# Performance work log

Measured on AMD Instinct MI355X. Metric: run time of the kernel, lower is better.

Reference implementation:

```python
import jax, jax.numpy as jnp
import numpy as np

TEMP = 0.5   # temperature from __init__
EPS = 1e-8   # torch.nn.CosineSimilarity eps


def setup_inputs() -> dict:
    key = jax.random.key(0)
    N, D = 8192, 256
    x = jax.random.normal(key, (N, D), dtype=jnp.float32)
    # pairs: each label appears exactly twice, as required for the
    # sim[~mask].reshape(N, -1) in the original to be well-formed
    y = jnp.arange(N, dtype=jnp.int32) // 2
    return {"x": x, "y": y}


def reference(x, y):
    # cosine similarity matrix: normalize once, then one NxD @ DxN matmul
    # (equivalent to CosineSimilarity(x.unsqueeze(1), x.unsqueeze(0)) without
    #  the NxNxD intermediate)
    norm = jnp.maximum(jnp.linalg.norm(x, axis=1, keepdims=True), EPS)
    xn = x / norm
    sim = (xn @ xn.T) / TEMP                     # [N, N]

    # Original: positives = equal-label entries (row-major order, includes the
    # diagonal), logits = [positives | negatives] which is just a per-row
    # permutation of sim; labels = 0 -> CE target is the FIRST equal-label
    # column of each row. logsumexp is over the full row (all N entries).
    eq = y[:, None] == y[None, :]                # [N, N] bool
    first_pos = jnp.argmax(eq, axis=1)           # first column j with y_j == y_i
    target = jnp.take_along_axis(sim, first_pos[:, None], axis=1)[:, 0]  # [N]

    lse = jax.nn.logsumexp(sim, axis=1)          # [N]
    N = x.shape[0]
    loss = jnp.sum(lse - target) / N             # CrossEntropyLoss(sum) / N
    return loss
```

## Files before the change

### kernel.cpp

```cpp
#include <hip/hip_runtime.h>
#include <hip/hip_bf16.h>

#define D 256
#define INV_TEMP 2.0f

typedef __attribute__((ext_vector_type(8))) short short8;
typedef __attribute__((ext_vector_type(4))) float floatx4;

__device__ __forceinline__ unsigned short f2bf(float f) {
    union { float f; unsigned u; } a; a.f = f;
    unsigned r = (a.u + 0x7fffu + ((a.u >> 16) & 1u)) >> 16;
    return (unsigned short)r;
}

__device__ __forceinline__ void gload_lds16(const unsigned short* g,
                                            unsigned short* l) {
    __builtin_amdgcn_global_load_lds(
        (const __attribute__((address_space(1))) unsigned int*)g,
        (__attribute__((address_space(3))) unsigned int*)l, 16, 0, 0);
}

__global__ void nt_prep_kernel(const float* __restrict__ x,
                               unsigned short* __restrict__ xnb,
                               float* __restrict__ pair_dot,
                               float* __restrict__ gsum,
                               unsigned int* __restrict__ gcnt) {
    if (blockIdx.x == 0 && threadIdx.x == 0) { *gsum = 0.f; *gcnt = 0u; }
    int p    = blockIdx.x * 4 + (threadIdx.x >> 6);
    int lane = threadIdx.x & 63;
    const float4* a4 = (const float4*)(x + (size_t)(2 * p) * D);
    const float4* b4 = (const float4*)(x + (size_t)(2 * p + 1) * D);
    float4 a = a4[lane], b = b4[lane];
    float saa = a.x * a.x + a.y * a.y + a.z * a.z + a.w * a.w;
    float sbb = b.x * b.x + b.y * b.y + b.z * b.z + b.w * b.w;
    float sab = a.x * b.x + a.y * b.y + a.z * b.z + a.w * b.w;
    #pragma unroll
    for (int off = 32; off; off >>= 1) {
        saa += __shfl_xor(saa, off);
        sbb += __shfl_xor(sbb, off);
        sab += __shfl_xor(sab, off);
    }
    float inva = 1.0f / fmaxf(sqrtf(saa), 1e-8f);
    float invb = 1.0f / fmaxf(sqrtf(sbb), 1e-8f);
    ushort4 oa, ob;
    oa.x = f2bf(a.x * inva); oa.y = f2bf(a.y * inva);
    oa.z = f2bf(a.z * inva); oa.w = f2bf(a.w * inva);
    ob.x = f2bf(b.x * invb); ob.y = f2bf(b.y * invb);
    ob.z = f2bf(b.z * invb); ob.w = f2bf(b.w * invb);
    ((ushort4*)(xnb + (size_t)(2 * p) * D))[lane] = oa;
    ((ushort4*)(xnb + (size_t)(2 * p + 1) * D))[lane] = ob;
    if (lane == 0)
        pair_dot[p] = sab * inva * invb * INV_TEMP;
}

__global__ __launch_bounds__(256, 2)
void nt_simexp_kernel(const unsigned short* __restrict__ xnb,
                      float* __restrict__ contrib) {
    __shared__ __align__(16) unsigned short Bs[128 * 256];

    const int p  = blockIdx.x >> 4, q = blockIdx.x & 15;
    const int s1 = 63 - p;
    const int c0 = 64 - p;
    const int q0 = (p + q) & 15;

    const int tid  = threadIdx.x;
    const int wave = tid >> 6, lane = tid & 63;
    const int wm   = wave & 1, wn = wave >> 1;
    const int quad = lane >> 4, c = lane & 15;

    auto strip_of = [&](int i) { return (i < c0) ? p : s1; };
    auto bi_of    = [&](int i) { return (i < c0) ? (p + i) : (s1 + i - c0); };

    auto load_B = [&](int bj) {
        const unsigned short* src = xnb + (size_t)(bj * 128) * D;
        int rs = lane >> 5, pp = lane & 31;
        #pragma unroll
        for (int t = 0; t < 16; ++t) {
            int wl = wave * 16 + t;
            int rr = wl * 2 + rs;
            int j  = (pp & ~7) | ((pp ^ rr) & 7);
            gload_lds16(src + (size_t)rr * D + j * 8, Bs + wl * 512 + lane * 8);
        }
    };

    short8 abuf[2][4], bbuf[2][4];

    auto load_a = [&](short8* dst, int bi, int ph) {
        const unsigned short* src = xnb + (size_t)(bi * 128 + wm * 64 + c) * D
                                        + ph * 32 + quad * 8;
        #pragma unroll
        for (int mt = 0; mt < 4; ++mt)
            dst[mt] = *(const short8*)(src + mt * 16 * D);
    };
    auto load_b = [&](short8* dst, int ph) {
        const int jg = ph * 4 + quad;
        const int pB = (jg & ~7) | ((jg ^ c) & 7);
        #pragma unroll
        for (int nt = 0; nt < 4; ++nt)
            dst[nt] = *(const short8*)(Bs + (wn * 64 + nt * 16 + c) * D + pB * 8);
    };

    floatx4 acc[4][4];

    int bj = strip_of(q0);
    load_B(bj);
    load_a(abuf[0], bi_of(q0), 0);
    __syncthreads();
    load_b(bbuf[0], 0);

    for (int i = q0; i < 65; i += 16) {
        const int bi = bi_of(i);
        const int ni = i + 16;
        const bool have_next = (ni < 65);
        const int nbj = have_next ? strip_of(ni) : -1;
        const bool same = have_next && (nbj == bj);

        #pragma unroll
        for (int mt = 0; mt < 4; ++mt)
            #pragma unroll
            for (int nt = 0; nt < 4; ++nt)
                acc[mt][nt] = (floatx4){0.f, 0.f, 0.f, 0.f};

        #pragma unroll
        for (int ph = 0; ph < 8; ++ph) {
            const int cur = ph & 1, nxt = cur ^ 1;
            if (ph < 7) {
                load_a(abuf[nxt], bi, ph + 1);
                load_b(bbuf[nxt], ph + 1);
            } else if (same) {
                load_a(abuf[0], bi_of(ni), 0);
                load_b(bbuf[0], 0);
            }
            #pragma unroll
            for (int mt = 0; mt < 4; ++mt)
                #pragma unroll
                for (int nt = 0; nt < 4; ++nt)
                    acc[mt][nt] = __builtin_amdgcn_mfma_f32_16x16x32_bf16(
                        abuf[cur][mt], bbuf[cur][nt], acc[mt][nt], 0, 0, 0);
        }

        if (have_next && !same) {
            __syncthreads();
            load_B(nbj);
            load_a(abuf[0], bi_of(ni), 0);
        }

        #pragma unroll
        for (int mt = 0; mt < 4; ++mt)
            #pragma unroll
            for (int nt = 0; nt < 4; ++nt)
                #pragma unroll
                for (int r = 0; r < 4; ++r)
                    acc[mt][nt][r] = __expf(acc[mt][nt][r] * INV_TEMP);

        #pragma unroll
        for (int mt = 0; mt < 4; ++mt) {
            float ps[4] = {0.f, 0.f, 0.f, 0.f};
            #pragma unroll
            for (int nt = 0; nt < 4; ++nt)
                #pragma unroll
                for (int r = 0; r < 4; ++r)
                    ps[r] += acc[mt][nt][r];
            #pragma unroll
            for (int off = 1; off < 16; off <<= 1)
                #pragma unroll
                for (int r = 0; r < 4; ++r)
                    ps[r] += __shfl_xor(ps[r], off);
            if (c == 0) {
                float4 v = {ps[0], ps[1], ps[2], ps[3]};
                *(float4*)(contrib + (((size_t)bi * 64 + bj) * 2 + wn) * 128 +
                           wm * 64 + mt * 16 + quad * 4) = v;
            }
        }
        if (bi != bj) {
            #pragma unroll
            for (int nt = 0; nt < 4; ++nt) {
                float cs = 0.f;
                #pragma unroll
                for (int mt = 0; mt < 4; ++mt)
                    #pragma unroll
                    for (int r = 0; r < 4; ++r)
                        cs += acc[mt][nt][r];
                cs += __shfl_xor(cs, 16);
                cs += __shfl_xor(cs, 32);
                if (quad == 0)
                    contrib[(((size_t)bj * 64 + bi) * 2 + wm) * 128 +
                            wn * 64 + nt * 16 + c] = cs;
            }
        }
        if (have_next && !same) {
            __syncthreads();
            bj = nbj;
            load_b(bbuf[0], 0);
        }
    }
}

__global__ void nt_reduce_kernel(const float* __restrict__ contrib,
                                 const float* __restrict__ pair_dot,
                                 float* __restrict__ gsum,
                                 unsigned int* __restrict__ gcnt,
                                 float* __restrict__ out, int N) {
    __shared__ float sm[256];
    __shared__ __align__(16) float rs[2][128];
    int b  = blockIdx.x;
    int jp = threadIdx.x & 3;
    int idx = threadIdx.x >> 2;
    int h  = idx >> 5, rg = idx & 31;
    const float* base = contrib + (((size_t)b * 64 + jp) * 2 + h) * 128 + rg * 4;
    float4 s = {0.f, 0.f, 0.f, 0.f};
    #pragma unroll
    for (int j16 = 0; j16 < 16; ++j16) {
        float4 v = *(const float4*)(base + (size_t)j16 * 1024);
        s.x += v.x; s.y += v.y; s.z += v.z; s.w += v.w;
    }
    #pragma unroll
    for (int off = 1; off < 4; off <<= 1) {
        s.x += __shfl_xor(s.x, off);
        s.y += __shfl_xor(s.y, off);
        s.z += __shfl_xor(s.z, off);
        s.w += __shfl_xor(s.w, off);
    }
    if (jp == 0) {
        float4 v = {s.x, s.y, s.z, s.w};
        *(float4*)&rs[h][rg * 4] = v;
    }
    __syncthreads();
    float v = 0.f;
    int rl = threadIdx.x & 127;
    if (threadIdx.x < 128) v = logf(rs[0][rl] + rs[1][rl]);
    else if (rl < 64)      v = -pair_dot[b * 64 + rl];
    sm[threadIdx.x] = v;
    __syncthreads();
    for (int st = 128; st; st >>= 1) {
        if ((int)threadIdx.x < st) sm[threadIdx.x] += sm[threadIdx.x + st];
        __syncthreads();
    }
    if (threadIdx.x == 0) {
        atomicAdd(gsum, sm[0]);
        __threadfence();
        if (atomicAdd(gcnt, 1u) == 63u) {
            __threadfence();
            float tot = atomicAdd(gsum, 0.0f);
            out[0] = (tot - (float)N) / (float)N;
        }
    }
}

extern "C" void kernel_launch(void* const* d_in, const int* in_sizes, int n_in,
                              void* d_out, int out_size, void* d_ws, size_t ws_size,
                              hipStream_t stream) {
    const float* x = (const float*)d_in[0];
    int N = in_sizes[0] / D;

    char* ws = (char*)d_ws;
    unsigned short* xnb = (unsigned short*)ws;
    float* pair_dot  = (float*)(ws + (size_t)N * D * 2);
    float* contrib   = pair_dot + N / 2;
    float* gsum      = contrib + (size_t)64 * 64 * 2 * 128;
    unsigned int* gcnt = (unsigned int*)(gsum + 1);

    nt_prep_kernel<<<N / 8, 256, 0, stream>>>(x, xnb, pair_dot, gsum, gcnt);
    nt_simexp_kernel<<<512, 256, 0, stream>>>(xnb, contrib);
    nt_reduce_kernel<<<N / 128, 256, 0, stream>>>(contrib, pair_dot, gsum, gcnt,
                                                  (float*)d_out, N);
}
```

Baseline: 113.8 us.

## Stage A tiles through LDS with a 4-deep async pipeline and 256-row blocks

The sim-exp kernel now uses 512-thread blocks that compute 256x128 tiles. A-operand k-slices are staged into a 4-buffer LDS ring via global_load_lds with a swizzled layout, replacing direct per-wave global loads, and explicit vmcnt waits plus barriers overlap loads with MFMA. The triangular tile schedule is rebuilt for 256-row A tiles, and the diagonal is handled per 128-row half. MFMA sections get raised wave priority. The intent is better reuse of A across waves and hidden load latency, at the cost of more LDS (occupancy), more barriers, and a larger grid granularity of 256 blocks.

```diff
diff --git a/kernel.cpp b/kernel.cpp
--- a/kernel.cpp
+++ b/kernel.cpp
@@ -53,67 +53,89 @@
         pair_dot[p] = sab * inva * invb * INV_TEMP;
 }
 
-__global__ __launch_bounds__(256, 2)
+__global__ __launch_bounds__(512, 2)
 void nt_simexp_kernel(const unsigned short* __restrict__ xnb,
                       float* __restrict__ contrib) {
     __shared__ __align__(16) unsigned short Bs[128 * 256];
-
-    const int p  = blockIdx.x >> 4, q = blockIdx.x & 15;
-    const int s1 = 63 - p;
-    const int c0 = 64 - p;
-    const int q0 = (p + q) & 15;
+    __shared__ __align__(16) unsigned short As[4][256 * 32];
+
+    const int p  = blockIdx.x >> 3, q = blockIdx.x & 7;
+    const int n0 = 32 - (p >> 1);
+    const int q0 = (p + q) & 7;
 
     const int tid  = threadIdx.x;
     const int wave = tid >> 6, lane = tid & 63;
-    const int wm   = wave & 1, wn = wave >> 1;
+    const int wm   = wave & 3, wn = wave >> 2;
     const int quad = lane >> 4, c = lane & 15;
-
-    auto strip_of = [&](int i) { return (i < c0) ? p : s1; };
-    auto bi_of    = [&](int i) { return (i < c0) ? (p + i) : (s1 + i - c0); };
+    const int pA   = quad ^ ((c >> 1) & 3);
+
+    auto bj_of = [&](int t) { return (t < n0) ? p : 63 - p; };
+    auto a_of  = [&](int t) { return (t < n0) ? (p >> 1) + t
+                                              : ((63 - p) >> 1) + (t - n0); };
 
     auto load_B = [&](int bj) {
         const unsigned short* src = xnb + (size_t)(bj * 128) * D;
         int rs = lane >> 5, pp = lane & 31;
         #pragma unroll
-        for (int t = 0; t < 16; ++t) {
-            int wl = wave * 16 + t;
+        for (int t = 0; t < 8; ++t) {
+            int wl = wave * 8 + t;
             int rr = wl * 2 + rs;
             int j  = (pp & ~7) | ((pp ^ rr) & 7);
             gload_lds16(src + (size_t)rr * D + j * 8, Bs + wl * 512 + lane * 8);
         }
     };
-
-    short8 abuf[2][4], bbuf[2][4];
-
-    auto load_a = [&](short8* dst, int bi, int ph) {
-        const unsigned short* src = xnb + (size_t)(bi * 128 + wm * 64 + c) * D
-                                        + ph * 32 + quad * 8;
-        #pragma unroll
-        for (int mt = 0; mt < 4; ++mt)
-            dst[mt] = *(const short8*)(src + mt * 16 * D);
+    auto load_A = [&](int a, int ph, unsigned short* Ab) {
+        const unsigned short* src = xnb + (size_t)(a * 256) * D + ph * 32;
+        int rl = lane >> 2, pq = lane & 3;
+        #pragma unroll
+        for (int t = 0; t < 2; ++t) {
+            int wl = wave * 2 + t;
+            int rr = wl * 16 + rl;
+            int j  = pq ^ ((rr >> 1) & 3);
+            gload_lds16(src + (size_t)rr * D + j * 8, Ab + wl * 512 + lane * 8);
+        }
     };
-    auto load_b = [&](short8* dst, int ph) {
+
+    floatx4 acc[4][4];
+    auto compute = [&](const unsigned short* Ab, int ph) {
+        short8 af[4], bf[4];
+        #pragma unroll
+        for (int mt = 0; mt < 4; ++mt)
+            af[mt] = *(const short8*)(Ab + (wm * 64 + mt * 16 + c) * 32 + pA * 8);
         const int jg = ph * 4 + quad;
         const int pB = (jg & ~7) | ((jg ^ c) & 7);
         #pragma unroll
         for (int nt = 0; nt < 4; ++nt)
-            dst[nt] = *(const short8*)(Bs + (wn * 64 + nt * 16 + c) * D + pB * 8);
+            bf[nt] = *(const short8*)(Bs + (wn * 64 + nt * 16 + c) * 256 + pB * 8);
+        __builtin_amdgcn_s_setprio(1);
+        #pragma unroll
+        for (int mt = 0; mt < 4; ++mt)
+            #pragma unroll
+            for (int nt = 0; nt < 4; ++nt)
+                acc[mt][nt] = __builtin_amdgcn_mfma_f32_16x16x32_bf16(
+                    af[mt], bf[nt], acc[mt][nt], 0, 0, 0);
+        __builtin_amdgcn_s_setprio(0);
     };
 
-    floatx4 acc[4][4];
-
-    int bj = strip_of(q0);
+    int t0 = q0;
+    int bj = bj_of(t0);
     load_B(bj);
-    load_a(abuf[0], bi_of(q0), 0);
-    __syncthreads();
-    load_b(bbuf[0], 0);
-
-    for (int i = q0; i < 65; i += 16) {
-        const int bi = bi_of(i);
-        const int ni = i + 16;
-        const bool have_next = (ni < 65);
-        const int nbj = have_next ? strip_of(ni) : -1;
-        const bool same = have_next && (nbj == bj);
+    {
+        int a0 = a_of(t0);
+        load_A(a0, 0, As[0]);
+        load_A(a0, 1, As[1]);
+        load_A(a0, 2, As[2]);
+    }
+    asm volatile("s_waitcnt vmcnt(4)" ::: "memory");
+    __builtin_amdgcn_s_barrier();
+    asm volatile("" ::: "memory");
+
+    for (int t = t0; t < 33; t += 8) {
+        const int a  = a_of(t);
+        const int tn = t + 8;
+        const bool have_next = (tn < 33);
+        const int a_next  = have_next ? a_of(tn) : 0;
+        const int bj_next = have_next ? bj_of(tn) : -1;
 
         #pragma unroll
         for (int mt = 0; mt < 4; ++mt)
@@ -122,28 +144,23 @@
                 acc[mt][nt] = (floatx4){0.f, 0.f, 0.f, 0.f};
 
         #pragma unroll
-        for (int ph = 0; ph < 8; ++ph) {
-            const int cur = ph & 1, nxt = cur ^ 1;
-            if (ph < 7) {
-                load_a(abuf[nxt], bi, ph + 1);
-                load_b(bbuf[nxt], ph + 1);
-            } else if (same) {
-                load_a(abuf[0], bi_of(ni), 0);
-                load_b(bbuf[0], 0);
+        for (int lp = 0; lp < 8; ++lp) {
+            if (lp < 5)           load_A(a,      lp + 3, As[(lp + 3) & 3]);
+            else if (have_next)   load_A(a_next, lp - 5, As[(lp + 3) & 3]);
+
+            compute(As[lp & 3], lp);
+
+            if (lp < 5 || have_next) {
+                asm volatile("s_waitcnt vmcnt(4)" ::: "memory");
+            } else if (lp < 7) {
+                asm volatile("s_waitcnt vmcnt(0)" ::: "memory");
             }
-            #pragma unroll
-            for (int mt = 0; mt < 4; ++mt)
-                #pragma unroll
-                for (int nt = 0; nt < 4; ++nt)
-                    acc[mt][nt] = __builtin_amdgcn_mfma_f32_16x16x32_bf16(
-                        abuf[cur][mt], bbuf[cur][nt], acc[mt][nt], 0, 0, 0);
-        }
-
-        if (have_next && !same) {
-            __syncthreads();
-            load_B(nbj);
-            load_a(abuf[0], bi_of(ni), 0);
-        }
+            __builtin_amdgcn_s_barrier();
+            asm volatile("" ::: "memory");
+        }
+
+        const int bi128 = 2 * a + (wm >> 1);
+        const int hrow  = wm & 1;
 
         #pragma unroll
         for (int mt = 0; mt < 4; ++mt)
@@ -153,26 +170,29 @@
                 for (int r = 0; r < 4; ++r)
                     acc[mt][nt][r] = __expf(acc[mt][nt][r] * INV_TEMP);
 
-        #pragma unroll
-        for (int mt = 0; mt < 4; ++mt) {
-            float ps[4] = {0.f, 0.f, 0.f, 0.f};
-            #pragma unroll
-            for (int nt = 0; nt < 4; ++nt)
-                #pragma unroll
-                for (int r = 0; r < 4; ++r)
-                    ps[r] += acc[mt][nt][r];
-            #pragma unroll
-            for (int off = 1; off < 16; off <<= 1)
-                #pragma unroll
-                for (int r = 0; r < 4; ++r)
-                    ps[r] += __shfl_xor(ps[r], off);
-            if (c == 0) {
-                float4 v = {ps[0], ps[1], ps[2], ps[3]};
-                *(float4*)(contrib + (((size_t)bi * 64 + bj) * 2 + wn) * 128 +
-                           wm * 64 + mt * 16 + quad * 4) = v;
+        if (bi128 >= bj) {
+            #pragma unroll
+            for (int mt = 0; mt < 4; ++mt) {
+                float ps[4] = {0.f, 0.f, 0.f, 0.f};
+                #pragma unroll
+                for (int nt = 0; nt < 4; ++nt)
+                    #pragma unroll
+                    for (int r = 0; r < 4; ++r)
+                        ps[r] += acc[mt][nt][r];
+                #pragma unroll
+                for (int off = 1; off < 16; off <<= 1)
+                    #pragma unroll
+                    for (int r = 0; r < 4; ++r)
+                        ps[r] += __shfl_xor(ps[r], off);
+                if (c == 0) {
+                    float4 v = {ps[0], ps[1], ps[2], ps[3]};
+                    *(float4*)(contrib +
+                        (((size_t)bi128 * 64 + bj) * 2 + wn) * 128 +
+                        hrow * 64 + mt * 16 + quad * 4) = v;
+                }
             }
         }
-        if (bi != bj) {
+        if (bi128 > bj) {
             #pragma unroll
             for (int nt = 0; nt < 4; ++nt) {
                 float cs = 0.f;
@@ -184,14 +204,17 @@
                 cs += __shfl_xor(cs, 16);
                 cs += __shfl_xor(cs, 32);
                 if (quad == 0)
-                    contrib[(((size_t)bj * 64 + bi) * 2 + wm) * 128 +
+                    contrib[(((size_t)bj * 64 + bi128) * 2 + hrow) * 128 +
                             wn * 64 + nt * 16 + c] = cs;
             }
         }
-        if (have_next && !same) {
-            __syncthreads();
-            bj = nbj;
-            load_b(bbuf[0], 0);
+
+        if (have_next && bj_next != bj) {
+            load_B(bj_next);
+            asm volatile("s_waitcnt vmcnt(0)" ::: "memory");
+            __builtin_amdgcn_s_barrier();
+            asm volatile("" ::: "memory");
+            bj = bj_next;
         }
     }
 }
@@ -261,7 +284,7 @@
     unsigned int* gcnt = (unsigned int*)(gsum + 1);
 
     nt_prep_kernel<<<N / 8, 256, 0, stream>>>(x, xnb, pair_dot, gsum, gcnt);
-    nt_simexp_kernel<<<512, 256, 0, stream>>>(xnb, contrib);
+    nt_simexp_kernel<<<256, 512, 0, stream>>>(xnb, contrib);
     nt_reduce_kernel<<<N / 128, 256, 0, stream>>>(contrib, pair_dot, gsum, gcnt,
                                                   (float*)d_out, N);
 }
```

Result: faster. 105.7 us (-7.1%).

## Replace LDS-tiled symmetric GEMM with single-wave register-resident 64-row tiles

Applied to the files above, without the earlier changes.

The similarity kernel is restructured so that each one-wave workgroup processes a 64x64 tile of the lower triangle. The whole A tile (64 rows by 256) stays in registers and B fragments stream straight from global memory with a three-deep prefetch, which removes LDS staging and barriers entirely. The grid grows to 2048 small blocks, MFMA issue is wrapped in s_setprio, and the contribution layout and the reduce kernel change to 128x128 tiles of 64 rows. In exchange, B data is no longer shared through LDS, so global and L2 traffic per MFMA rises, and the 32 short8 A fragments held per lane push up VGPR pressure.

```diff
diff --git a/kernel.cpp b/kernel.cpp
--- a/kernel.cpp
+++ b/kernel.cpp
@@ -11,13 +11,6 @@
     union { float f; unsigned u; } a; a.f = f;
     unsigned r = (a.u + 0x7fffu + ((a.u >> 16) & 1u)) >> 16;
     return (unsigned short)r;
-}
-
-__device__ __forceinline__ void gload_lds16(const unsigned short* g,
-                                            unsigned short* l) {
-    __builtin_amdgcn_global_load_lds(
-        (const __attribute__((address_space(1))) unsigned int*)g,
-        (__attribute__((address_space(3))) unsigned int*)l, 16, 0, 0);
 }
 
 __global__ void nt_prep_kernel(const float* __restrict__ x,
@@ -53,196 +46,158 @@
         pair_dot[p] = sab * inva * invb * INV_TEMP;
 }
 
-__global__ __launch_bounds__(256, 2)
+__global__ __launch_bounds__(64, 2)
 void nt_simexp_kernel(const unsigned short* __restrict__ xnb,
-                      float* __restrict__ contrib) {
-    __shared__ __align__(16) unsigned short Bs[128 * 256];
-
-    const int p  = blockIdx.x >> 4, q = blockIdx.x & 15;
-    const int s1 = 63 - p;
-    const int c0 = 64 - p;
-    const int q0 = (p + q) & 15;
-
-    const int tid  = threadIdx.x;
-    const int wave = tid >> 6, lane = tid & 63;
-    const int wm   = wave & 1, wn = wave >> 1;
+                      float* __restrict__ contrib2) {
+    const int pairIdx = blockIdx.x >> 5;
+    const int w       = blockIdx.x & 31;
+    const int i0 = pairIdx, i1 = 127 - pairIdx;
+    const int cnt0 = i0 + 1;
+
+    const int lane = threadIdx.x & 63;
     const int quad = lane >> 4, c = lane & 15;
-
-    auto strip_of = [&](int i) { return (i < c0) ? p : s1; };
-    auto bi_of    = [&](int i) { return (i < c0) ? (p + i) : (s1 + i - c0); };
-
-    auto load_B = [&](int bj) {
-        const unsigned short* src = xnb + (size_t)(bj * 128) * D;
-        int rs = lane >> 5, pp = lane & 31;
-        #pragma unroll
-        for (int t = 0; t < 16; ++t) {
-            int wl = wave * 16 + t;
-            int rr = wl * 2 + rs;
-            int j  = (pp & ~7) | ((pp ^ rr) & 7);
-            gload_lds16(src + (size_t)rr * D + j * 8, Bs + wl * 512 + lane * 8);
-        }
-    };
-
-    short8 abuf[2][4], bbuf[2][4];
-
-    auto load_a = [&](short8* dst, int bi, int ph) {
-        const unsigned short* src = xnb + (size_t)(bi * 128 + wm * 64 + c) * D
-                                        + ph * 32 + quad * 8;
+    const size_t lane_off = (size_t)c * D + quad * 8;
+
+    short8 af[4][8];
+    int cur_i = -1;
+
+    for (int m = w; m < 129; m += 32) {
+        const int on0 = (m < cnt0);
+        const int i = on0 ? i0 : i1;
+        const int j = on0 ? m : (m - cnt0);
+
+        if (i != cur_i) {
+            cur_i = i;
+            const unsigned short* ab = xnb + (size_t)i * 64 * D + lane_off;
+            #pragma unroll
+            for (int mt = 0; mt < 4; ++mt)
+                #pragma unroll
+                for (int ph = 0; ph < 8; ++ph)
+                    af[mt][ph] = *(const short8*)(ab + (size_t)mt * 16 * D + ph * 32);
+        }
+
+        const unsigned short* bb = xnb + (size_t)j * 64 * D + lane_off;
+        auto loadB = [&](int s, short8* dst) {
+            const int h = s >> 3, ph = s & 7;
+            const unsigned short* src = bb + (size_t)(h * 32) * D + ph * 32;
+            dst[0] = *(const short8*)(src);
+            dst[1] = *(const short8*)(src + (size_t)16 * D);
+        };
+
+        short8 bf[4][2];
+        loadB(0, bf[0]);
+        loadB(1, bf[1]);
+        loadB(2, bf[2]);
+
+        float rps[4][4];
         #pragma unroll
         for (int mt = 0; mt < 4; ++mt)
-            dst[mt] = *(const short8*)(src + mt * 16 * D);
-    };
-    auto load_b = [&](short8* dst, int ph) {
-        const int jg = ph * 4 + quad;
-        const int pB = (jg & ~7) | ((jg ^ c) & 7);
-        #pragma unroll
-        for (int nt = 0; nt < 4; ++nt)
-            dst[nt] = *(const short8*)(Bs + (wn * 64 + nt * 16 + c) * D + pB * 8);
-    };
-
-    floatx4 acc[4][4];
-
-    int bj = strip_of(q0);
-    load_B(bj);
-    load_a(abuf[0], bi_of(q0), 0);
-    __syncthreads();
-    load_b(bbuf[0], 0);
-
-    for (int i = q0; i < 65; i += 16) {
-        const int bi = bi_of(i);
-        const int ni = i + 16;
-        const bool have_next = (ni < 65);
-        const int nbj = have_next ? strip_of(ni) : -1;
-        const bool same = have_next && (nbj == bj);
-
-        #pragma unroll
-        for (int mt = 0; mt < 4; ++mt)
-            #pragma unroll
-            for (int nt = 0; nt < 4; ++nt)
-                acc[mt][nt] = (floatx4){0.f, 0.f, 0.f, 0.f};
-
-        #pragma unroll
-        for (int ph = 0; ph < 8; ++ph) {
-            const int cur = ph & 1, nxt = cur ^ 1;
-            if (ph < 7) {
-                load_a(abuf[nxt], bi, ph + 1);
-                load_b(bbuf[nxt], ph + 1);
-            } else if (same) {
-                load_a(abuf[0], bi_of(ni), 0);
-                load_b(bbuf[0], 0);
-            }
-            #pragma unroll
-            for (int mt = 0; mt < 4; ++mt)
-                #pragma unroll
-                for (int nt = 0; nt < 4; ++nt)
-                    acc[mt][nt] = __builtin_amdgcn_mfma_f32_16x16x32_bf16(
-                        abuf[cur][mt], bbuf[cur][nt], acc[mt][nt], 0, 0, 0);
-        }
-
-        if (have_next && !same) {
-            __syncthreads();
-            load_B(nbj);
-            load_a(abuf[0], bi_of(ni), 0);
-        }
-
-        #pragma unroll
-        for (int mt = 0; mt < 4; ++mt)
-            #pragma unroll
-            for (int nt = 0; nt < 4; ++nt)
-                #pragma unroll
-                for (int r = 0; r < 4; ++r)
-                    acc[mt][nt][r] = __expf(acc[mt][nt][r] * INV_TEMP);
-
-        #pragma unroll
-        for (int mt = 0; mt < 4; ++mt) {
-            float ps[4] = {0.f, 0.f, 0.f, 0.f};
-            #pragma unroll
-            for (int nt = 0; nt < 4; ++nt)
-                #pragma unroll
-                for (int r = 0; r < 4; ++r)
-                    ps[r] += acc[mt][nt][r];
-            #pragma unroll
-            for (int off = 1; off < 16; off <<= 1)
-                #pragma unroll
-                for (int r = 0; r < 4; ++r)
-                    ps[r] += __shfl_xor(ps[r], off);
-            if (c == 0) {
-                float4 v = {ps[0], ps[1], ps[2], ps[3]};
-                *(float4*)(contrib + (((size_t)bi * 64 + bj) * 2 + wn) * 128 +
-                           wm * 64 + mt * 16 + quad * 4) = v;
-            }
-        }
-        if (bi != bj) {
-            #pragma unroll
-            for (int nt = 0; nt < 4; ++nt) {
-                float cs = 0.f;
+            #pragma unroll
+            for (int r = 0; r < 4; ++r)
+                rps[mt][r] = 0.f;
+
+        floatx4 acc[4][2];
+
+        #pragma unroll
+        for (int s = 0; s < 16; ++s) {
+            const int h = s >> 3, ph = s & 7;
+            if (ph == 0) {
                 #pragma unroll
                 for (int mt = 0; mt < 4; ++mt)
                     #pragma unroll
-                    for (int r = 0; r < 4; ++r)
-                        cs += acc[mt][nt][r];
-                cs += __shfl_xor(cs, 16);
-                cs += __shfl_xor(cs, 32);
-                if (quad == 0)
-                    contrib[(((size_t)bj * 64 + bi) * 2 + wm) * 128 +
-                            wn * 64 + nt * 16 + c] = cs;
-            }
-        }
-        if (have_next && !same) {
-            __syncthreads();
-            bj = nbj;
-            load_b(bbuf[0], 0);
+                    for (int nt = 0; nt < 2; ++nt)
+                        acc[mt][nt] = (floatx4){0.f, 0.f, 0.f, 0.f};
+            }
+            if (s + 3 < 16) loadB(s + 3, bf[(s + 3) & 3]);
+
+            __builtin_amdgcn_s_setprio(1);
+            #pragma unroll
+            for (int mt = 0; mt < 4; ++mt)
+                #pragma unroll
+                for (int nt = 0; nt < 2; ++nt)
+                    acc[mt][nt] = __builtin_amdgcn_mfma_f32_16x16x32_bf16(
+                        af[mt][ph], bf[s & 3][nt], acc[mt][nt], 0, 0, 0);
+            __builtin_amdgcn_s_setprio(0);
+
+            if (ph == 7) {
+                #pragma unroll
+                for (int mt = 0; mt < 4; ++mt)
+                    #pragma unroll
+                    for (int nt = 0; nt < 2; ++nt)
+                        #pragma unroll
+                        for (int r = 0; r < 4; ++r) {
+                            float e = __expf(acc[mt][nt][r] * INV_TEMP);
+                            acc[mt][nt][r] = e;
+                            rps[mt][r] += e;
+                        }
+                if (j < i) {
+                    #pragma unroll
+                    for (int nt = 0; nt < 2; ++nt) {
+                        float cs = 0.f;
+                        #pragma unroll
+                        for (int mt = 0; mt < 4; ++mt)
+                            #pragma unroll
+                            for (int r = 0; r < 4; ++r)
+                                cs += acc[mt][nt][r];
+                        cs += __shfl_xor(cs, 16);
+                        cs += __shfl_xor(cs, 32);
+                        if (quad == 0)
+                            contrib2[((size_t)j * 128 + i) * 64 +
+                                     h * 32 + nt * 16 + c] = cs;
+                    }
+                }
+            }
+        }
+
+        #pragma unroll
+        for (int mt = 0; mt < 4; ++mt) {
+            float p0 = rps[mt][0], p1 = rps[mt][1];
+            float p2 = rps[mt][2], p3 = rps[mt][3];
+            #pragma unroll
+            for (int off = 1; off < 16; off <<= 1) {
+                p0 += __shfl_xor(p0, off);
+                p1 += __shfl_xor(p1, off);
+                p2 += __shfl_xor(p2, off);
+                p3 += __shfl_xor(p3, off);
+            }
+            if (c == 0) {
+                float4 v = {p0, p1, p2, p3};
+                *(float4*)(contrib2 + ((size_t)i * 128 + j) * 64 +
+                           mt * 16 + quad * 4) = v;
+            }
         }
     }
 }
 
-__global__ void nt_reduce_kernel(const float* __restrict__ contrib,
+__global__ void nt_reduce_kernel(const float* __restrict__ contrib2,
                                  const float* __restrict__ pair_dot,
                                  float* __restrict__ gsum,
                                  unsigned int* __restrict__ gcnt,
                                  float* __restrict__ out, int N) {
     __shared__ float sm[256];
-    __shared__ __align__(16) float rs[2][128];
-    int b  = blockIdx.x;
-    int jp = threadIdx.x & 3;
-    int idx = threadIdx.x >> 2;
-    int h  = idx >> 5, rg = idx & 31;
-    const float* base = contrib + (((size_t)b * 64 + jp) * 2 + h) * 128 + rg * 4;
-    float4 s = {0.f, 0.f, 0.f, 0.f};
+    int i  = blockIdx.x;
+    int r  = threadIdx.x & 63, jp = threadIdx.x >> 6;
+    float s = 0.f;
+    const float* base = contrib2 + ((size_t)i * 128 + jp) * 64 + r;
     #pragma unroll
-    for (int j16 = 0; j16 < 16; ++j16) {
-        float4 v = *(const float4*)(base + (size_t)j16 * 1024);
-        s.x += v.x; s.y += v.y; s.z += v.z; s.w += v.w;
-    }
-    #pragma unroll
-    for (int off = 1; off < 4; off <<= 1) {
-        s.x += __shfl_xor(s.x, off);
-        s.y += __shfl_xor(s.y, off);
-        s.z += __shfl_xor(s.z, off);
-        s.w += __shfl_xor(s.w, off);
-    }
-    if (jp == 0) {
-        float4 v = {s.x, s.y, s.z, s.w};
-        *(float4*)&rs[h][rg * 4] = v;
-    }
+    for (int jj = 0; jj < 32; ++jj)
+        s += base[(size_t)jj * 4 * 64];
+    sm[threadIdx.x] = s;
     __syncthreads();
-    float v = 0.f;
-    int rl = threadIdx.x & 127;
-    if (threadIdx.x < 128) v = logf(rs[0][rl] + rs[1][rl]);
-    else if (rl < 64)      v = -pair_dot[b * 64 + rl];
-    sm[threadIdx.x] = v;
-    __syncthreads();
-    for (int st = 128; st; st >>= 1) {
-        if ((int)threadIdx.x < st) sm[threadIdx.x] += sm[threadIdx.x + st];
-        __syncthreads();
-    }
-    if (threadIdx.x == 0) {
-        atomicAdd(gsum, sm[0]);
-        __threadfence();
-        if (atomicAdd(gcnt, 1u) == 63u) {
+    if (threadIdx.x < 64) {
+        float tot = sm[r] + sm[64 + r] + sm[128 + r] + sm[192 + r];
+        float v = logf(tot);
+        if (!(r & 1)) v -= pair_dot[i * 32 + (r >> 1)];
+        #pragma unroll
+        for (int off = 32; off; off >>= 1) v += __shfl_xor(v, off);
+        if (r == 0) {
+            atomicAdd(gsum, v);
             __threadfence();
-            float tot = atomicAdd(gsum, 0.0f);
-            out[0] = (tot - (float)N) / (float)N;
+            if (atomicAdd(gcnt, 1u) == 127u) {
+                __threadfence();
+                float t = atomicAdd(gsum, 0.0f);
+                out[0] = (t - (float)N) / (float)N;
+            }
         }
     }
 }
@@ -256,12 +211,12 @@
     char* ws = (char*)d_ws;
     unsigned short* xnb = (unsigned short*)ws;
     float* pair_dot  = (float*)(ws + (size_t)N * D * 2);
-    float* contrib   = pair_dot + N / 2;
-    float* gsum      = contrib + (size_t)64 * 64 * 2 * 128;
+    float* contrib2  = pair_dot + N / 2;
+    float* gsum      = contrib2 + (size_t)128 * 128 * 64;
     unsigned int* gcnt = (unsigned int*)(gsum + 1);
 
     nt_prep_kernel<<<N / 8, 256, 0, stream>>>(x, xnb, pair_dot, gsum, gcnt);
-    nt_simexp_kernel<<<512, 256, 0, stream>>>(xnb, contrib);
-    nt_reduce_kernel<<<N / 128, 256, 0, stream>>>(contrib, pair_dot, gsum, gcnt,
-                                                  (float*)d_out, N);
-}
+    nt_simexp_kernel<<<2048, 64, 0, stream>>>(xnb, contrib2);
+    nt_reduce_kernel<<<128, 256, 0, stream>>>(contrib2, pair_dot, gsum, gcnt,
+                                              (float*)d_out, N);
+}
```

New measurement: 119.9 us. +5.3%, slower.
